# Kernel tuning notes

Measured on AMD Instinct MI355X. Metric: run time of the kernel, lower is better.

## Reference

```python
import jax, jax.numpy as jnp
import numpy as np

N = 100000   # nodes (batched graph)
E = 1600000  # edges
G = 2048     # molecules in the batch
D_IN = 128
D_H = 128
MLP_H = 512


def setup_inputs() -> dict:
    key = jax.random.key(0)
    ks = jax.random.split(key, 20)

    def w(k, i, o):
        return (jax.random.normal(k, (i, o), jnp.float32) / np.sqrt(i)).astype(jnp.float32)

    feats = jax.random.normal(ks[0], (N, D_IN), jnp.float32)
    src = jax.random.randint(ks[1], (E,), 0, N)
    dst = jax.random.randint(ks[2], (E,), 0, N)
    graph_ids = jnp.sort(jax.random.randint(ks[3], (N,), 0, G))

    return {
        "feats": feats, "src": src, "dst": dst, "graph_ids": graph_ids,
        # 3 GraphConv layers
        "W0": w(ks[4], D_IN, D_H), "b0": jnp.zeros((D_H,), jnp.float32),
        "W1": w(ks[5], D_H, D_H),  "b1": jnp.zeros((D_H,), jnp.float32),
        "W2": w(ks[6], D_H, D_H),  "b2": jnp.zeros((D_H,), jnp.float32),
        # MLP head: D_H -> 512 -> 256 -> 1
        "Wm0": w(ks[7], D_H, MLP_H),       "bm0": jnp.zeros((MLP_H,), jnp.float32),
        "Wm1": w(ks[8], MLP_H, MLP_H // 2), "bm1": jnp.zeros((MLP_H // 2,), jnp.float32),
        "Wm2": w(ks[9], MLP_H // 2, 1),     "bm2": jnp.zeros((1,), jnp.float32),
    }


def reference(feats, src, dst, graph_ids, W0, b0, W1, b1, W2, b2,
              Wm0, bm0, Wm1, bm1, Wm2, bm2):
    ones_e = jnp.ones((E,), jnp.float32)
    # DGL GraphConv norm='both': D_out^{-1/2} on src, D_in^{-1/2} on dst; deg clamped to 1
    deg_out = jnp.maximum(jax.ops.segment_sum(ones_e, src, num_segments=N), 1.0)
    deg_in = jnp.maximum(jax.ops.segment_sum(ones_e, dst, num_segments=N), 1.0)
    inv_src = jax.lax.rsqrt(deg_out)[:, None]
    inv_dst = jax.lax.rsqrt(deg_in)[:, None]

    def gcn_layer(h, W, b):
        h = h * inv_src                                   # [N, D]
        m = jax.ops.segment_sum(h[src], dst, num_segments=N)  # gather-scatter over edges
        m = m * inv_dst
        return jax.nn.relu(jnp.dot(m, W) + b)

    h = gcn_layer(feats, W0, b0)
    h = gcn_layer(h, W1, b1)
    h = gcn_layer(h, W2, b2)

    # AvgPooling per graph
    counts = jnp.maximum(jax.ops.segment_sum(jnp.ones((N,), jnp.float32), graph_ids, num_segments=G), 1.0)
    emb = jax.ops.segment_sum(h, graph_ids, num_segments=G) / counts[:, None]  # [G, D_H]

    # MLP head (dropout = identity in eval)
    x = jax.nn.relu(jnp.dot(emb, Wm0) + bm0)
    x = jax.nn.relu(jnp.dot(x, Wm1) + bm1)
    return jnp.dot(x, Wm2) + bm2  # [G, 1]
```

## Files before the change

### kernel.cpp

```cpp
#include <hip/hip_runtime.h>


static inline int ceil_div(int a, int b){ return (a + b - 1) / b; }

#define B1 256
#define NBMAX 1024

typedef __bf16 bf16x8 __attribute__((ext_vector_type(8)));
typedef float  f32x4  __attribute__((ext_vector_type(4)));

static __device__ inline __bf16 bits_to_bf16(unsigned short u){
  union { unsigned short u; __bf16 b; } x; x.u = u; return x.b;
}
static __device__ inline unsigned short bf16_bits(__bf16 b){
  union { __bf16 b; unsigned short u; } x; x.b = b; return x.u;
}
static __device__ inline unsigned pack_split(float s){
  __bf16 h = (__bf16)s;
  __bf16 l = (__bf16)(s - (float)h);
  return ((unsigned)bf16_bits(h) << 16) | (unsigned)bf16_bits(l);
}

__global__ __launch_bounds__(256) void bucket_count_kernel(
    const int* __restrict__ src, const int* __restrict__ dst,
    unsigned* __restrict__ cntA, unsigned* __restrict__ cntB,
    int E, int NB){
  __shared__ unsigned la[NBMAX], lb[NBMAX];
  int t = threadIdx.x;
  for (int i = t; i < NB; i += 256){ la[i] = 0u; lb[i] = 0u; }
  __syncthreads();
  int chunk = (E + B1 - 1) / B1;
  int e0 = blockIdx.x * chunk, e1 = min(e0 + chunk, E);
  for (int e = e0 + t; e < e1; e += 256){
    atomicAdd(&la[dst[e] >> 7], 1u);
    atomicAdd(&lb[src[e] >> 7], 1u);
  }
  __syncthreads();
  for (int i = t; i < NB; i += 256){
    cntA[(size_t)blockIdx.x * NB + i] = la[i];
    cntB[(size_t)blockIdx.x * NB + i] = lb[i];
  }
}

__global__ void scan_cols_kernel(unsigned* __restrict__ cntA, unsigned* __restrict__ cntB,
                                 unsigned* __restrict__ totals, int NB){
  int b = blockIdx.x * 256 + threadIdx.x;
  if (b >= NB) return;
  unsigned* cnt = blockIdx.y ? cntB : cntA;
  unsigned run = 0;
  for (int blk = 0; blk < B1; blk++){
    unsigned v = cnt[(size_t)blk * NB + b];
    cnt[(size_t)blk * NB + b] = run;
    run += v;
  }
  totals[(size_t)blockIdx.y * NB + b] = run;
}

__global__ void scan_base_kernel(const unsigned* __restrict__ totals,
                                 unsigned* __restrict__ baseA, unsigned* __restrict__ baseB,
                                 int NB, int E){
  __shared__ unsigned s[NBMAX];
  int t = threadIdx.x;
  for (int job = 0; job < 2; job++){
    unsigned* base = job ? baseB : baseA;
    unsigned x = (t < NB) ? totals[(size_t)job * NB + t] : 0u;
    s[t] = x;
    __syncthreads();
    for (int off = 1; off < NBMAX; off <<= 1){
      unsigned v = (t >= off) ? s[t - off] : 0u;
      __syncthreads();
      s[t] += v;
      __syncthreads();
    }
    if (t < NB) base[t] = s[t] - x;
    if (t == 0) base[NB] = (unsigned)E;
    __syncthreads();
  }
}

__global__ __launch_bounds__(256) void bucket_scatter_kernel(
    const int* __restrict__ src, const int* __restrict__ dst,
    const unsigned* __restrict__ cntA, const unsigned* __restrict__ cntB,
    const unsigned* __restrict__ baseA, const unsigned* __restrict__ baseB,
    unsigned* __restrict__ bpack_d, unsigned char* __restrict__ bsrc_s,
    int E, int NB){
  __shared__ unsigned curA[NBMAX], curB[NBMAX];
  int t = threadIdx.x;
  for (int i = t; i < NB; i += 256){
    curA[i] = baseA[i] + cntA[(size_t)blockIdx.x * NB + i];
    curB[i] = baseB[i] + cntB[(size_t)blockIdx.x * NB + i];
  }
  __syncthreads();
  int chunk = (E + B1 - 1) / B1;
  int e0 = blockIdx.x * chunk, e1 = min(e0 + chunk, E);
  for (int e = e0 + t; e < e1; e += 256){
    int s = src[e], d = dst[e];
    unsigned p = atomicAdd(&curA[d >> 7], 1u);
    bpack_d[p] = ((unsigned)(d & 127) << 17) | (unsigned)s;
    unsigned q = atomicAdd(&curB[s >> 7], 1u);
    bsrc_s[q] = (unsigned char)(s & 127);
  }
}

__global__ __launch_bounds__(256) void csr_finalize_kernel(
    const unsigned* __restrict__ bpack_d, const unsigned char* __restrict__ bsrc_s,
    const unsigned* __restrict__ baseA, const unsigned* __restrict__ baseB,
    int* __restrict__ row_ptr, float* __restrict__ inv_dst, float* __restrict__ inv_src,
    int* __restrict__ col, int N, int E, int NB){
  __shared__ unsigned cnt[128];
  __shared__ unsigned scn[128];
  int b = blockIdx.x, t = threadIdx.x;
  int node0 = b << 7;
  int nn = min(128, N - node0);
  int e0 = (int)baseA[b], e1 = (int)baseA[b + 1];
  if (t < 128) cnt[t] = 0u;
  __syncthreads();
  for (int e = e0 + t; e < e1; e += 256)
    atomicAdd(&cnt[(bpack_d[e] >> 17) & 127u], 1u);
  __syncthreads();
  unsigned mycnt = (t < 128) ? cnt[t] : 0u;
  if (t < 128) scn[t] = mycnt;
  __syncthreads();
  for (int off = 1; off < 128; off <<= 1){
    unsigned v = (t < 128 && t >= off) ? scn[t - off] : 0u;
    __syncthreads();
    if (t < 128) scn[t] += v;
    __syncthreads();
  }
  if (t < nn){
    unsigned excl = scn[t] - mycnt;
    row_ptr[node0 + t] = e0 + (int)excl;
    unsigned c = mycnt < 1u ? 1u : mycnt;
    inv_dst[node0 + t] = rsqrtf((float)c);
    cnt[t] = (unsigned)e0 + excl;
  }
  if (b == NB - 1 && t == 0) row_ptr[N] = E;
  __syncthreads();
  for (int e = e0 + t; e < e1; e += 256){
    unsigned v = bpack_d[e];
    unsigned p = atomicAdd(&cnt[(v >> 17) & 127u], 1u);
    col[p] = (int)(v & 0x1FFFFu);
  }
  __syncthreads();
  if (t < 128) cnt[t] = 0u;
  __syncthreads();
  int f0 = (int)baseB[b], f1 = (int)baseB[b + 1];
  for (int e = f0 + t; e < f1; e += 256)
    atomicAdd(&cnt[bsrc_s[e]], 1u);
  __syncthreads();
  if (t < nn){
    unsigned c = cnt[t] < 1u ? 1u : cnt[t];
    inv_src[node0 + t] = rsqrtf((float)c);
  }
}

template<bool SC>
__global__ __launch_bounds__(256) void csr_agg_kernel(
    const int* __restrict__ row_ptr, const int* __restrict__ col,
    const float* __restrict__ hs, const float* __restrict__ scale,
    const float* __restrict__ inv_dst, unsigned* __restrict__ aggp, int N){
  int node = (int)((blockIdx.x*256u + threadIdx.x) >> 5);
  int lane = threadIdx.x & 31;
  if (node >= N) return;
  int r0 = row_ptr[node];
  int r1 = row_ptr[node+1];
  float4 a0 = make_float4(0.f,0.f,0.f,0.f);
  float4 a1 = make_float4(0.f,0.f,0.f,0.f);
  float4 a2 = make_float4(0.f,0.f,0.f,0.f);
  float4 a3 = make_float4(0.f,0.f,0.f,0.f);
  int e = r0;
  for (; e + 3 < r1; e += 4){
    int s0 = col[e], s1 = col[e+1], s2 = col[e+2], s3 = col[e+3];
    float4 v0 = ((const float4*)(hs + (size_t)s0*128))[lane];
    float4 v1 = ((const float4*)(hs + (size_t)s1*128))[lane];
    float4 v2 = ((const float4*)(hs + (size_t)s2*128))[lane];
    float4 v3 = ((const float4*)(hs + (size_t)s3*128))[lane];
    if (SC){
      float c0 = scale[s0], c1 = scale[s1], c2 = scale[s2], c3 = scale[s3];
      v0.x*=c0; v0.y*=c0; v0.z*=c0; v0.w*=c0;
      v1.x*=c1; v1.y*=c1; v1.z*=c1; v1.w*=c1;
      v2.x*=c2; v2.y*=c2; v2.z*=c2; v2.w*=c2;
      v3.x*=c3; v3.y*=c3; v3.z*=c3; v3.w*=c3;
    }
    a0.x += v0.x; a0.y += v0.y; a0.z += v0.z; a0.w += v0.w;
    a1.x += v1.x; a1.y += v1.y; a1.z += v1.z; a1.w += v1.w;
    a2.x += v2.x; a2.y += v2.y; a2.z += v2.z; a2.w += v2.w;
    a3.x += v3.x; a3.y += v3.y; a3.z += v3.z; a3.w += v3.w;
  }
  for (; e < r1; e++){
    int s0 = col[e];
    float4 v0 = ((const float4*)(hs + (size_t)s0*128))[lane];
    if (SC){ float c0 = scale[s0]; v0.x*=c0; v0.y*=c0; v0.z*=c0; v0.w*=c0; }
    a0.x += v0.x; a0.y += v0.y; a0.z += v0.z; a0.w += v0.w;
  }
  float idst = inv_dst[node];
  float rx = ((a0.x + a1.x) + (a2.x + a3.x)) * idst;
  float ry = ((a0.y + a1.y) + (a2.y + a3.y)) * idst;
  float rz = ((a0.z + a1.z) + (a2.z + a3.z)) * idst;
  float rw = ((a0.w + a1.w) + (a2.w + a3.w)) * idst;
  uint4 p;
  p.x = pack_split(rx); p.y = pack_split(ry);
  p.z = pack_split(rz); p.w = pack_split(rw);
  ((uint4*)(aggp + (size_t)node*128))[lane] = p;
}

__global__ void wprep_kernel(const float* __restrict__ W0, const float* __restrict__ W1,
                             const float* __restrict__ W2,
                             __bf16* __restrict__ Wsp){
  int gidx = blockIdx.x*256 + threadIdx.x;
  if (gidx >= 3*128*128) return;
  int layer = gidx >> 14, idx = gidx & 16383;
  const float* W = layer == 0 ? W0 : (layer == 1 ? W1 : W2);
  int k = idx >> 7, n = idx & 127;
  float w = W[idx];
  __bf16 h = (__bf16)w;
  __bf16 l = (__bf16)(w - (float)h);
  Wsp[(size_t)layer*2*16384 + n*128 + k] = h;
  Wsp[(size_t)layer*2*16384 + 16384 + n*128 + k] = l;
}

__global__ __launch_bounds__(256) void mfma_gemm_kernel(
    const unsigned* __restrict__ A,
    const __bf16* __restrict__ Whi, const __bf16* __restrict__ Wlo,
    const float* __restrict__ bias, const float* __restrict__ out_scale,
    float* __restrict__ out, int M){
  const int tid  = threadIdx.x;
  const int wv   = tid >> 6;
  const int lane = tid & 63;
  const int q    = lane >> 4;
  const int mn   = lane & 15;
  const int row0 = blockIdx.x*128 + wv*32;

  f32x4 acc[2][8];
  #pragma unroll
  for (int mt = 0; mt < 2; mt++)
    #pragma unroll
    for (int nt = 0; nt < 8; nt++)
      acc[mt][nt] = (f32x4){0.f,0.f,0.f,0.f};

  #pragma unroll
  for (int kc = 0; kc < 4; kc++){
    bf16x8 ah[2], al[2];
    #pragma unroll
    for (int mt = 0; mt < 2; mt++){
      const unsigned* ap = A + (size_t)(row0 + mt*16 + mn)*128 + kc*32 + q*8;
      uint4 x0 = *(const uint4*)ap;
      uint4 x1 = *(const uint4*)(ap + 4);
      unsigned v[8] = {x0.x, x0.y, x0.z, x0.w, x1.x, x1.y, x1.z, x1.w};
      #pragma unroll
      for (int j = 0; j < 8; j++){
        ah[mt][j] = bits_to_bf16((unsigned short)(v[j] >> 16));
        al[mt][j] = bits_to_bf16((unsigned short)(v[j] & 0xFFFFu));
      }
    }
    #pragma unroll
    for (int nt = 0; nt < 8; nt++){
      size_t boff = (size_t)(nt*16 + mn)*128 + kc*32 + q*8;
      bf16x8 bh = *(const bf16x8*)(Whi + boff);
      bf16x8 bl = *(const bf16x8*)(Wlo + boff);
      #pragma unroll
      for (int mt = 0; mt < 2; mt++){
        acc[mt][nt] = __builtin_amdgcn_mfma_f32_16x16x32_bf16(al[mt], bh, acc[mt][nt], 0, 0, 0);
        acc[mt][nt] = __builtin_amdgcn_mfma_f32_16x16x32_bf16(ah[mt], bl, acc[mt][nt], 0, 0, 0);
        acc[mt][nt] = __builtin_amdgcn_mfma_f32_16x16x32_bf16(ah[mt], bh, acc[mt][nt], 0, 0, 0);
      }
    }
  }

  #pragma unroll
  for (int mt = 0; mt < 2; mt++){
    #pragma unroll
    for (int r = 0; r < 4; r++){
      int gm = row0 + mt*16 + q*4 + r;
      if (gm < M){
        float osc = out_scale ? out_scale[gm] : 1.f;
        #pragma unroll
        for (int nt = 0; nt < 8; nt++){
          float v = acc[mt][nt][r] + bias[nt*16 + mn];
          v = fmaxf(v, 0.f) * osc;
          out[(size_t)gm*128 + nt*16 + mn] = v;
        }
      }
    }
  }
}

__global__ __launch_bounds__(256) void gemm_kernel(
    const float* __restrict__ A, const float* __restrict__ W,
    const float* __restrict__ bias, const float* __restrict__ row_scale,
    const float* __restrict__ out_scale, float* __restrict__ out,
    int M, int K, int Ncols, int do_relu){
  __shared__ float As[32][68];
  __shared__ float Bs[32][128];

  const int tid = threadIdx.x;
  const int tx = tid & 31;
  const int ty = tid >> 5;
  const int row0 = blockIdx.x * 64;
  const int col0 = blockIdx.y * 128;

  float acc[8][4];
  #pragma unroll
  for (int i = 0; i < 8; i++)
    #pragma unroll
    for (int j = 0; j < 4; j++) acc[i][j] = 0.f;

  for (int kb = 0; kb < K; kb += 32){
    #pragma unroll
    for (int i = 0; i < 2; i++){
      int flat = i*256 + tid;
      int m = flat >> 3, k4 = (flat & 7) << 2;
      int gm = row0 + m;
      float4 v = make_float4(0.f, 0.f, 0.f, 0.f);
      if (gm < M){
        v = *(const float4*)(A + (size_t)gm*K + kb + k4);
        if (row_scale){ float s = row_scale[gm]; v.x*=s; v.y*=s; v.z*=s; v.w*=s; }
      }
      As[k4+0][m] = v.x; As[k4+1][m] = v.y; As[k4+2][m] = v.z; As[k4+3][m] = v.w;
    }
    #pragma unroll
    for (int i = 0; i < 4; i++){
      int flat = i*256 + tid;
      int k = flat >> 5, j4 = (flat & 31) << 2;
      float4 v = *(const float4*)(W + (size_t)(kb + k)*Ncols + col0 + j4);
      *(float4*)&Bs[k][j4] = v;
    }
    __syncthreads();
    #pragma unroll
    for (int k = 0; k < 32; k++){
      float4 b = *(const float4*)&Bs[k][tx << 2];
      float a[8];
      #pragma unroll
      for (int i = 0; i < 8; i++) a[i] = As[k][ty*8 + i];
      #pragma unroll
      for (int i = 0; i < 8; i++){
        acc[i][0] = fmaf(a[i], b.x, acc[i][0]);
        acc[i][1] = fmaf(a[i], b.y, acc[i][1]);
        acc[i][2] = fmaf(a[i], b.z, acc[i][2]);
        acc[i][3] = fmaf(a[i], b.w, acc[i][3]);
      }
    }
    __syncthreads();
  }

  float4 bi = *(const float4*)(bias + col0 + (tx << 2));
  #pragma unroll
  for (int i = 0; i < 8; i++){
    int gm = row0 + ty*8 + i;
    if (gm < M){
      float4 v;
      v.x = acc[i][0] + bi.x; v.y = acc[i][1] + bi.y;
      v.z = acc[i][2] + bi.z; v.w = acc[i][3] + bi.w;
      if (do_relu){
        v.x = fmaxf(v.x, 0.f); v.y = fmaxf(v.y, 0.f);
        v.z = fmaxf(v.z, 0.f); v.w = fmaxf(v.w, 0.f);
      }
      if (out_scale){ float s = out_scale[gm]; v.x*=s; v.y*=s; v.z*=s; v.w*=s; }
      *(float4*)(out + (size_t)gm*Ncols + col0 + (tx << 2)) = v;
    }
  }
}

__global__ void pool_kernel(const float* __restrict__ h, const int* __restrict__ gid,
                            float* __restrict__ emb, int N, int G){
  int g = blockIdx.x;
  int lane = threadIdx.x;
  int lo = 0, hi = N;
  while (lo < hi){ int mid = (lo + hi) >> 1; if (gid[mid] < g) lo = mid + 1; else hi = mid; }
  int start = lo;
  hi = N;
  while (lo < hi){ int mid = (lo + hi) >> 1; if (gid[mid] <= g) lo = mid + 1; else hi = mid; }
  int end = lo;
  float ax = 0.f, ay = 0.f;
  for (int n = start; n < end; n++){
    float2 v = ((const float2*)(h + (size_t)n*128))[lane];
    ax += v.x; ay += v.y;
  }
  int c = end - start; if (c < 1) c = 1;
  float invc = 1.0f / (float)c;
  float2 r; r.x = ax * invc; r.y = ay * invc;
  ((float2*)(emb + (size_t)g*128))[lane] = r;
}

__global__ void final_dot_kernel(const float* __restrict__ x, const float* __restrict__ w,
                                 const float* __restrict__ b, float* __restrict__ out, int G){
  int idx = blockIdx.x*blockDim.x + threadIdx.x;
  int g = idx >> 6, lane = idx & 63;
  if (g >= G) return;
  float4 xv = ((const float4*)(x + (size_t)g*256))[lane];
  float4 wv = ((const float4*)w)[lane];
  float s = xv.x*wv.x + xv.y*wv.y + xv.z*wv.z + xv.w*wv.w;
  for (int off = 32; off > 0; off >>= 1) s += __shfl_down(s, off);
  if (lane == 0) out[g] = s + b[0];
}

extern "C" void kernel_launch(void* const* d_in, const int* in_sizes, int n_in,
                              void* d_out, int out_size, void* d_ws, size_t ws_size,
                              hipStream_t stream){
  const float* feats = (const float*)d_in[0];
  const int*   src   = (const int*)d_in[1];
  const int*   dst   = (const int*)d_in[2];
  const int*   gid   = (const int*)d_in[3];
  const float* W0 = (const float*)d_in[4];   const float* b0 = (const float*)d_in[5];
  const float* W1 = (const float*)d_in[6];   const float* b1 = (const float*)d_in[7];
  const float* W2 = (const float*)d_in[8];   const float* b2 = (const float*)d_in[9];
  const float* Wm0 = (const float*)d_in[10]; const float* bm0 = (const float*)d_in[11];
  const float* Wm1 = (const float*)d_in[12]; const float* bm1 = (const float*)d_in[13];
  const float* Wm2 = (const float*)d_in[14]; const float* bm2 = (const float*)d_in[15];
  float* out = (float*)d_out;

  const int E   = in_sizes[1];
  const int N   = in_sizes[3];
  const int G   = out_size;
  const int MH  = in_sizes[11];
  const int MH2 = in_sizes[13];
  const int NB  = ceil_div(N, 128);

  char* ws = (char*)d_ws;
  size_t off = 0;
  auto carve = [&](size_t bytes) -> char* {
    off = (off + 255) & ~(size_t)255;
    char* p = ws + off; off += bytes; return p;
  };
  float* inv_src = (float*)carve((size_t)N*4);
  float* inv_dst = (float*)carve((size_t)N*4);
  int* row_ptr = (int*)carve((size_t)(N+1)*4);
  int* col     = (int*)carve((size_t)E*4);
  __bf16* Wsp = (__bf16*)carve(6*128*128*2);
  float* hs  = (float*)carve((size_t)N*128*4);
  unsigned* aggp = (unsigned*)carve((size_t)N*128*4);
  float* emb = (float*)carve((size_t)G*128*4);
  float* x1  = (float*)carve((size_t)G*MH*4);
  float* x2  = (float*)carve((size_t)G*MH2*4);

  unsigned* T = (unsigned*)aggp;
  unsigned* cntA   = T;
  unsigned* cntB   = cntA + (size_t)B1*NB;
  unsigned* totals = cntB + (size_t)B1*NB;
  unsigned* baseA  = totals + 2*(size_t)NB;
  unsigned* baseB  = baseA + (NB+1);
  unsigned* bpack_d = baseB + (NB+1);
  unsigned char* bsrc_s = (unsigned char*)(bpack_d + E);

  bucket_count_kernel<<<B1, 256, 0, stream>>>(src, dst, cntA, cntB, E, NB);
  scan_cols_kernel<<<dim3(ceil_div(NB,256), 2), 256, 0, stream>>>(cntA, cntB, totals, NB);
  scan_base_kernel<<<1, NBMAX, 0, stream>>>(totals, baseA, baseB, NB, E);
  bucket_scatter_kernel<<<B1, 256, 0, stream>>>(src, dst, cntA, cntB, baseA, baseB,
                                                bpack_d, bsrc_s, E, NB);
  csr_finalize_kernel<<<NB, 256, 0, stream>>>(bpack_d, bsrc_s, baseA, baseB,
                                              row_ptr, inv_dst, inv_src, col, N, E, NB);
  wprep_kernel<<<192, 256, 0, stream>>>(W0, W1, W2, Wsp);

  const int agg_blocks = ceil_div(N*32, 256);
  const int ggrid = ceil_div(N, 128);
  __bf16 *Whi0 = Wsp,            *Wlo0 = Wsp + 16384;
  __bf16 *Whi1 = Wsp + 2*16384,  *Wlo1 = Wsp + 3*16384;
  __bf16 *Whi2 = Wsp + 4*16384,  *Wlo2 = Wsp + 5*16384;
  csr_agg_kernel<true><<<agg_blocks, 256, 0, stream>>>(row_ptr, col, feats, inv_src, inv_dst, aggp, N);
  mfma_gemm_kernel<<<ggrid, 256, 0, stream>>>(aggp, Whi0, Wlo0, b0, inv_src, hs, N);
  csr_agg_kernel<false><<<agg_blocks, 256, 0, stream>>>(row_ptr, col, hs, nullptr, inv_dst, aggp, N);
  mfma_gemm_kernel<<<ggrid, 256, 0, stream>>>(aggp, Whi1, Wlo1, b1, inv_src, hs, N);
  csr_agg_kernel<false><<<agg_blocks, 256, 0, stream>>>(row_ptr, col, hs, nullptr, inv_dst, aggp, N);
  mfma_gemm_kernel<<<ggrid, 256, 0, stream>>>(aggp, Whi2, Wlo2, b2, nullptr, hs, N);
  pool_kernel<<<G, 64, 0, stream>>>(hs, gid, emb, N, G);
  gemm_kernel<<<dim3(ceil_div(G,64), MH/128),  256, 0, stream>>>(emb, Wm0, bm0, nullptr, nullptr, x1, G, 128, MH, 1);
  gemm_kernel<<<dim3(ceil_div(G,64), MH2/128), 256, 0, stream>>>(x1, Wm1, bm1, nullptr, nullptr, x2, G, MH, MH2, 1);
  final_dot_kernel<<<ceil_div(G*64,256), 256, 0, stream>>>(x2, Wm2, bm2, out, G);
}
```

Before: 789.7 us.

## Stage edge buckets in LDS per chunk and fuse pooling with MLP head

The count and scatter passes of CSR construction are merged into one kernel. Each block sorts its edge chunk into per-bucket order in shared memory and writes the staged chunk contiguously, and the finalize kernel reads each chunk's segment using the per-block offsets. Weight preparation rides along as extra blocks of that kernel, and pooling plus the three MLP layers become a single head kernel that handles 8 graphs per block. This removes several launches and one full pass over the edge list, at the cost of serial per-thread loops in finalize and a smaller, less parallel head GEMM.

```diff
diff --git a/kernel.cpp b/kernel.cpp
--- a/kernel.cpp
+++ b/kernel.cpp
@@ -5,6 +5,8 @@
 
 #define B1 256
 #define NBMAX 1024
+#define CHUNK_MAX 7168
+#define WPREP_BLOCKS 192
 
 typedef __bf16 bf16x8 __attribute__((ext_vector_type(8)));
 typedef float  f32x4  __attribute__((ext_vector_type(4)));
@@ -21,39 +23,105 @@
   return ((unsigned)bf16_bits(h) << 16) | (unsigned)bf16_bits(l);
 }
 
-__global__ __launch_bounds__(256) void bucket_count_kernel(
+__global__ __launch_bounds__(256) void scatter_count_kernel(
     const int* __restrict__ src, const int* __restrict__ dst,
     unsigned* __restrict__ cntA, unsigned* __restrict__ cntB,
+    unsigned* __restrict__ stagedA, unsigned char* __restrict__ stagedB,
+    const float* __restrict__ W0, const float* __restrict__ W1,
+    const float* __restrict__ W2, __bf16* __restrict__ Wsp,
     int E, int NB){
+  if (blockIdx.x >= B1){
+    int gidx = (blockIdx.x - B1)*256 + threadIdx.x;
+    if (gidx < 3*128*128){
+      int layer = gidx >> 14, idx = gidx & 16383;
+      const float* W = layer == 0 ? W0 : (layer == 1 ? W1 : W2);
+      int k = idx >> 7, n = idx & 127;
+      float w = W[idx];
+      __bf16 h = (__bf16)w;
+      __bf16 l = (__bf16)(w - (float)h);
+      Wsp[(size_t)layer*2*16384 + n*128 + k] = h;
+      Wsp[(size_t)layer*2*16384 + 16384 + n*128 + k] = l;
+    }
+    return;
+  }
+
   __shared__ unsigned la[NBMAX], lb[NBMAX];
-  int t = threadIdx.x;
-  for (int i = t; i < NB; i += 256){ la[i] = 0u; lb[i] = 0u; }
-  __syncthreads();
-  int chunk = (E + B1 - 1) / B1;
-  int e0 = blockIdx.x * chunk, e1 = min(e0 + chunk, E);
+  __shared__ unsigned tsum[256];
+  __shared__ unsigned stA[CHUNK_MAX];
+  __shared__ unsigned char stB[CHUNK_MAX];
+
+  const int t = threadIdx.x;
+  const int blk = blockIdx.x;
+  const int chunk = (E + B1 - 1) / B1;
+  const int e0 = blk * chunk, e1 = min(e0 + chunk, E);
+  const int len = e1 - e0;
+  const int strideB = (chunk + 3) & ~3;
+
+  #pragma unroll
+  for (int i = t; i < NBMAX; i += 256){ la[i] = 0u; lb[i] = 0u; }
+  __syncthreads();
   for (int e = e0 + t; e < e1; e += 256){
     atomicAdd(&la[dst[e] >> 7], 1u);
     atomicAdd(&lb[src[e] >> 7], 1u);
   }
   __syncthreads();
-  for (int i = t; i < NB; i += 256){
-    cntA[(size_t)blockIdx.x * NB + i] = la[i];
-    cntB[(size_t)blockIdx.x * NB + i] = lb[i];
-  }
-}
-
-__global__ void scan_cols_kernel(unsigned* __restrict__ cntA, unsigned* __restrict__ cntB,
-                                 unsigned* __restrict__ totals, int NB){
+
+  for (int job = 0; job < 2; job++){
+    unsigned* lx = job ? lb : la;
+    unsigned* cx = job ? cntB : cntA;
+    int b4 = t*4;
+    unsigned v0 = lx[b4], v1 = lx[b4+1], v2 = lx[b4+2], v3 = lx[b4+3];
+    unsigned s = v0+v1+v2+v3;
+    tsum[t] = s;
+    __syncthreads();
+    for (int off = 1; off < 256; off <<= 1){
+      unsigned u = (t >= off) ? tsum[t-off] : 0u;
+      __syncthreads();
+      tsum[t] += u;
+      __syncthreads();
+    }
+    unsigned run = tsum[t] - s;
+    unsigned o0 = run, o1 = run+v0, o2 = run+v0+v1, o3 = run+v0+v1+v2;
+    lx[b4] = o0; lx[b4+1] = o1; lx[b4+2] = o2; lx[b4+3] = o3;
+    if (b4   < NB) cx[(size_t)blk*NB + b4  ] = o0;
+    if (b4+1 < NB) cx[(size_t)blk*NB + b4+1] = o1;
+    if (b4+2 < NB) cx[(size_t)blk*NB + b4+2] = o2;
+    if (b4+3 < NB) cx[(size_t)blk*NB + b4+3] = o3;
+    __syncthreads();
+  }
+
+  for (int e = e0 + t; e < e1; e += 256){
+    int s = src[e], d = dst[e];
+    unsigned pA = atomicAdd(&la[d >> 7], 1u);
+    stA[pA] = ((unsigned)(d & 127) << 17) | (unsigned)s;
+    unsigned pB = atomicAdd(&lb[s >> 7], 1u);
+    stB[pB] = (unsigned char)(s & 127);
+  }
+  __syncthreads();
+
+  for (int i = t; i < len; i += 256)
+    stagedA[(size_t)blk*chunk + i] = stA[i];
+  int w4 = (len + 3) >> 2;
+  unsigned* gB = (unsigned*)(stagedB + (size_t)blk*strideB);
+  for (int i = t; i < w4; i += 256)
+    gB[i] = *(unsigned*)&stB[4*i];
+}
+
+__global__ void totals_kernel(const unsigned* __restrict__ cntA,
+                              const unsigned* __restrict__ cntB,
+                              unsigned* __restrict__ totals, int NB, int E){
   int b = blockIdx.x * 256 + threadIdx.x;
   if (b >= NB) return;
-  unsigned* cnt = blockIdx.y ? cntB : cntA;
+  const unsigned* cx = blockIdx.y ? cntB : cntA;
+  const int chunk = (E + B1 - 1) / B1;
   unsigned run = 0;
   for (int blk = 0; blk < B1; blk++){
-    unsigned v = cnt[(size_t)blk * NB + b];
-    cnt[(size_t)blk * NB + b] = run;
-    run += v;
-  }
-  totals[(size_t)blockIdx.y * NB + b] = run;
+    int lenb = E - blk*chunk; if (lenb > chunk) lenb = chunk; if (lenb < 0) lenb = 0;
+    unsigned cur = cx[(size_t)blk*NB + b];
+    unsigned nxt = (b < NB-1) ? cx[(size_t)blk*NB + b + 1] : (unsigned)lenb;
+    run += nxt - cur;
+  }
+  totals[(size_t)blockIdx.y*NB + b] = run;
 }
 
 __global__ void scan_base_kernel(const unsigned* __restrict__ totals,
@@ -63,7 +131,7 @@
   int t = threadIdx.x;
   for (int job = 0; job < 2; job++){
     unsigned* base = job ? baseB : baseA;
-    unsigned x = (t < NB) ? totals[(size_t)job * NB + t] : 0u;
+    unsigned x = (t < NB) ? totals[(size_t)job*NB + t] : 0u;
     s[t] = x;
     __syncthreads();
     for (int off = 1; off < NBMAX; off <<= 1){
@@ -78,45 +146,29 @@
   }
 }
 
-__global__ __launch_bounds__(256) void bucket_scatter_kernel(
-    const int* __restrict__ src, const int* __restrict__ dst,
+__global__ __launch_bounds__(256) void csr_finalize_kernel(
+    const unsigned* __restrict__ stagedA, const unsigned char* __restrict__ stagedB,
     const unsigned* __restrict__ cntA, const unsigned* __restrict__ cntB,
-    const unsigned* __restrict__ baseA, const unsigned* __restrict__ baseB,
-    unsigned* __restrict__ bpack_d, unsigned char* __restrict__ bsrc_s,
-    int E, int NB){
-  __shared__ unsigned curA[NBMAX], curB[NBMAX];
-  int t = threadIdx.x;
-  for (int i = t; i < NB; i += 256){
-    curA[i] = baseA[i] + cntA[(size_t)blockIdx.x * NB + i];
-    curB[i] = baseB[i] + cntB[(size_t)blockIdx.x * NB + i];
-  }
-  __syncthreads();
-  int chunk = (E + B1 - 1) / B1;
-  int e0 = blockIdx.x * chunk, e1 = min(e0 + chunk, E);
-  for (int e = e0 + t; e < e1; e += 256){
-    int s = src[e], d = dst[e];
-    unsigned p = atomicAdd(&curA[d >> 7], 1u);
-    bpack_d[p] = ((unsigned)(d & 127) << 17) | (unsigned)s;
-    unsigned q = atomicAdd(&curB[s >> 7], 1u);
-    bsrc_s[q] = (unsigned char)(s & 127);
-  }
-}
-
-__global__ __launch_bounds__(256) void csr_finalize_kernel(
-    const unsigned* __restrict__ bpack_d, const unsigned char* __restrict__ bsrc_s,
-    const unsigned* __restrict__ baseA, const unsigned* __restrict__ baseB,
+    const unsigned* __restrict__ baseA,
     int* __restrict__ row_ptr, float* __restrict__ inv_dst, float* __restrict__ inv_src,
     int* __restrict__ col, int N, int E, int NB){
   __shared__ unsigned cnt[128];
   __shared__ unsigned scn[128];
-  int b = blockIdx.x, t = threadIdx.x;
-  int node0 = b << 7;
-  int nn = min(128, N - node0);
-  int e0 = (int)baseA[b], e1 = (int)baseA[b + 1];
+  const int b = blockIdx.x, t = threadIdx.x;
+  const int node0 = b << 7;
+  const int nn = min(128, N - node0);
+  const int chunk = (E + B1 - 1) / B1;
+  const int strideB = (chunk + 3) & ~3;
+  int lenb = E - t*chunk; if (lenb > chunk) lenb = chunk; if (lenb < 0) lenb = 0;
+
+  const unsigned a0 = cntA[(size_t)t*NB + b];
+  const unsigned a1 = (b < NB-1) ? cntA[(size_t)t*NB + b + 1] : (unsigned)lenb;
+  const unsigned* segA = stagedA + (size_t)t*chunk;
+
   if (t < 128) cnt[t] = 0u;
   __syncthreads();
-  for (int e = e0 + t; e < e1; e += 256)
-    atomicAdd(&cnt[(bpack_d[e] >> 17) & 127u], 1u);
+  for (unsigned i = a0; i < a1; i++)
+    atomicAdd(&cnt[(segA[i] >> 17) & 127u], 1u);
   __syncthreads();
   unsigned mycnt = (t < 128) ? cnt[t] : 0u;
   if (t < 128) scn[t] = mycnt;
@@ -127,6 +179,7 @@
     if (t < 128) scn[t] += v;
     __syncthreads();
   }
+  int e0 = (int)baseA[b];
   if (t < nn){
     unsigned excl = scn[t] - mycnt;
     row_ptr[node0 + t] = e0 + (int)excl;
@@ -136,17 +189,19 @@
   }
   if (b == NB - 1 && t == 0) row_ptr[N] = E;
   __syncthreads();
-  for (int e = e0 + t; e < e1; e += 256){
-    unsigned v = bpack_d[e];
+  for (unsigned i = a0; i < a1; i++){
+    unsigned v = segA[i];
     unsigned p = atomicAdd(&cnt[(v >> 17) & 127u], 1u);
     col[p] = (int)(v & 0x1FFFFu);
   }
   __syncthreads();
   if (t < 128) cnt[t] = 0u;
   __syncthreads();
-  int f0 = (int)baseB[b], f1 = (int)baseB[b + 1];
-  for (int e = f0 + t; e < f1; e += 256)
-    atomicAdd(&cnt[bsrc_s[e]], 1u);
+  const unsigned b0o = cntB[(size_t)t*NB + b];
+  const unsigned b1o = (b < NB-1) ? cntB[(size_t)t*NB + b + 1] : (unsigned)lenb;
+  const unsigned char* segB = stagedB + (size_t)t*strideB;
+  for (unsigned i = b0o; i < b1o; i++)
+    atomicAdd(&cnt[segB[i]], 1u);
   __syncthreads();
   if (t < nn){
     unsigned c = cnt[t] < 1u ? 1u : cnt[t];
@@ -204,21 +259,6 @@
   ((uint4*)(aggp + (size_t)node*128))[lane] = p;
 }
 
-__global__ void wprep_kernel(const float* __restrict__ W0, const float* __restrict__ W1,
-                             const float* __restrict__ W2,
-                             __bf16* __restrict__ Wsp){
-  int gidx = blockIdx.x*256 + threadIdx.x;
-  if (gidx >= 3*128*128) return;
-  int layer = gidx >> 14, idx = gidx & 16383;
-  const float* W = layer == 0 ? W0 : (layer == 1 ? W1 : W2);
-  int k = idx >> 7, n = idx & 127;
-  float w = W[idx];
-  __bf16 h = (__bf16)w;
-  __bf16 l = (__bf16)(w - (float)h);
-  Wsp[(size_t)layer*2*16384 + n*128 + k] = h;
-  Wsp[(size_t)layer*2*16384 + 16384 + n*128 + k] = l;
-}
-
 __global__ __launch_bounds__(256) void mfma_gemm_kernel(
     const unsigned* __restrict__ A,
     const __bf16* __restrict__ Whi, const __bf16* __restrict__ Wlo,
@@ -285,113 +325,93 @@
   }
 }
 
-__global__ __launch_bounds__(256) void gemm_kernel(
-    const float* __restrict__ A, const float* __restrict__ W,
-    const float* __restrict__ bias, const float* __restrict__ row_scale,
-    const float* __restrict__ out_scale, float* __restrict__ out,
-    int M, int K, int Ncols, int do_relu){
-  __shared__ float As[32][68];
-  __shared__ float Bs[32][128];
-
-  const int tid = threadIdx.x;
-  const int tx = tid & 31;
-  const int ty = tid >> 5;
-  const int row0 = blockIdx.x * 64;
-  const int col0 = blockIdx.y * 128;
-
-  float acc[8][4];
-  #pragma unroll
-  for (int i = 0; i < 8; i++)
-    #pragma unroll
-    for (int j = 0; j < 4; j++) acc[i][j] = 0.f;
-
-  for (int kb = 0; kb < K; kb += 32){
-    #pragma unroll
-    for (int i = 0; i < 2; i++){
-      int flat = i*256 + tid;
-      int m = flat >> 3, k4 = (flat & 7) << 2;
-      int gm = row0 + m;
-      float4 v = make_float4(0.f, 0.f, 0.f, 0.f);
-      if (gm < M){
-        v = *(const float4*)(A + (size_t)gm*K + kb + k4);
-        if (row_scale){ float s = row_scale[gm]; v.x*=s; v.y*=s; v.z*=s; v.w*=s; }
+__global__ __launch_bounds__(256) void head_kernel(
+    const float* __restrict__ h, const int* __restrict__ gid,
+    const float* __restrict__ Wm0, const float* __restrict__ bm0,
+    const float* __restrict__ Wm1, const float* __restrict__ bm1,
+    const float* __restrict__ Wm2, const float* __restrict__ bm2,
+    float* __restrict__ out, int N, int G){
+  __shared__ float embL[8][128];
+  __shared__ float x1L[8][512];
+  __shared__ float x2L[8][256];
+
+  const int t = threadIdx.x;
+  const int wave = t >> 6, lane = t & 63;
+  const int g0 = blockIdx.x * 8;
+
+  for (int gg = 0; gg < 2; gg++){
+    int gl = wave*2 + gg;
+    int g = g0 + gl;
+    float ax = 0.f, ay = 0.f;
+    int start = 0, end = 0;
+    if (g < G){
+      int lo = 0, hi = N;
+      while (lo < hi){ int mid = (lo + hi) >> 1; if (gid[mid] < g) lo = mid + 1; else hi = mid; }
+      start = lo;
+      hi = N;
+      while (lo < hi){ int mid = (lo + hi) >> 1; if (gid[mid] <= g) lo = mid + 1; else hi = mid; }
+      end = lo;
+      for (int n = start; n < end; n++){
+        float2 v = ((const float2*)(h + (size_t)n*128))[lane];
+        ax += v.x; ay += v.y;
       }
-      As[k4+0][m] = v.x; As[k4+1][m] = v.y; As[k4+2][m] = v.z; As[k4+3][m] = v.w;
-    }
-    #pragma unroll
-    for (int i = 0; i < 4; i++){
-      int flat = i*256 + tid;
-      int k = flat >> 5, j4 = (flat & 31) << 2;
-      float4 v = *(const float4*)(W + (size_t)(kb + k)*Ncols + col0 + j4);
-      *(float4*)&Bs[k][j4] = v;
-    }
-    __syncthreads();
-    #pragma unroll
-    for (int k = 0; k < 32; k++){
-      float4 b = *(const float4*)&Bs[k][tx << 2];
-      float a[8];
+    }
+    int c = end - start; if (c < 1) c = 1;
+    float invc = 1.0f / (float)c;
+    embL[gl][2*lane]   = ax * invc;
+    embL[gl][2*lane+1] = ay * invc;
+  }
+  __syncthreads();
+
+  {
+    float acc[8][2];
+    #pragma unroll
+    for (int g = 0; g < 8; g++){ acc[g][0] = 0.f; acc[g][1] = 0.f; }
+    for (int k = 0; k < 128; k++){
+      float w0 = Wm0[(size_t)k*512 + t];
+      float w1 = Wm0[(size_t)k*512 + t + 256];
       #pragma unroll
-      for (int i = 0; i < 8; i++) a[i] = As[k][ty*8 + i];
+      for (int g = 0; g < 8; g++){
+        float e = embL[g][k];
+        acc[g][0] = fmaf(e, w0, acc[g][0]);
+        acc[g][1] = fmaf(e, w1, acc[g][1]);
+      }
+    }
+    float b0v = bm0[t], b1v = bm0[t + 256];
+    #pragma unroll
+    for (int g = 0; g < 8; g++){
+      x1L[g][t]       = fmaxf(acc[g][0] + b0v, 0.f);
+      x1L[g][t + 256] = fmaxf(acc[g][1] + b1v, 0.f);
+    }
+  }
+  __syncthreads();
+
+  {
+    float acc[8];
+    #pragma unroll
+    for (int g = 0; g < 8; g++) acc[g] = 0.f;
+    for (int k = 0; k < 512; k++){
+      float w = Wm1[(size_t)k*256 + t];
       #pragma unroll
-      for (int i = 0; i < 8; i++){
-        acc[i][0] = fmaf(a[i], b.x, acc[i][0]);
-        acc[i][1] = fmaf(a[i], b.y, acc[i][1]);
-        acc[i][2] = fmaf(a[i], b.z, acc[i][2]);
-        acc[i][3] = fmaf(a[i], b.w, acc[i][3]);
-      }
-    }
-    __syncthreads();
-  }
-
-  float4 bi = *(const float4*)(bias + col0 + (tx << 2));
-  #pragma unroll
-  for (int i = 0; i < 8; i++){
-    int gm = row0 + ty*8 + i;
-    if (gm < M){
-      float4 v;
-      v.x = acc[i][0] + bi.x; v.y = acc[i][1] + bi.y;
-      v.z = acc[i][2] + bi.z; v.w = acc[i][3] + bi.w;
-      if (do_relu){
-        v.x = fmaxf(v.x, 0.f); v.y = fmaxf(v.y, 0.f);
-        v.z = fmaxf(v.z, 0.f); v.w = fmaxf(v.w, 0.f);
-      }
-      if (out_scale){ float s = out_scale[gm]; v.x*=s; v.y*=s; v.z*=s; v.w*=s; }
-      *(float4*)(out + (size_t)gm*Ncols + col0 + (tx << 2)) = v;
-    }
-  }
-}
-
-__global__ void pool_kernel(const float* __restrict__ h, const int* __restrict__ gid,
-                            float* __restrict__ emb, int N, int G){
-  int g = blockIdx.x;
-  int lane = threadIdx.x;
-  int lo = 0, hi = N;
-  while (lo < hi){ int mid = (lo + hi) >> 1; if (gid[mid] < g) lo = mid + 1; else hi = mid; }
-  int start = lo;
-  hi = N;
-  while (lo < hi){ int mid = (lo + hi) >> 1; if (gid[mid] <= g) lo = mid + 1; else hi = mid; }
-  int end = lo;
-  float ax = 0.f, ay = 0.f;
-  for (int n = start; n < end; n++){
-    float2 v = ((const float2*)(h + (size_t)n*128))[lane];
-    ax += v.x; ay += v.y;
-  }
-  int c = end - start; if (c < 1) c = 1;
-  float invc = 1.0f / (float)c;
-  float2 r; r.x = ax * invc; r.y = ay * invc;
-  ((float2*)(emb + (size_t)g*128))[lane] = r;
-}
-
-__global__ void final_dot_kernel(const float* __restrict__ x, const float* __restrict__ w,
-                                 const float* __restrict__ b, float* __restrict__ out, int G){
-  int idx = blockIdx.x*blockDim.x + threadIdx.x;
-  int g = idx >> 6, lane = idx & 63;
-  if (g >= G) return;
-  float4 xv = ((const float4*)(x + (size_t)g*256))[lane];
-  float4 wv = ((const float4*)w)[lane];
-  float s = xv.x*wv.x + xv.y*wv.y + xv.z*wv.z + xv.w*wv.w;
-  for (int off = 32; off > 0; off >>= 1) s += __shfl_down(s, off);
-  if (lane == 0) out[g] = s + b[0];
+      for (int g = 0; g < 8; g++)
+        acc[g] = fmaf(x1L[g][k], w, acc[g]);
+    }
+    float bv = bm1[t];
+    #pragma unroll
+    for (int g = 0; g < 8; g++)
+      x2L[g][t] = fmaxf(acc[g] + bv, 0.f);
+  }
+  __syncthreads();
+
+  {
+    int g = t >> 5;
+    int c = t & 31;
+    float s = 0.f;
+    for (int i = c; i < 256; i += 32)
+      s = fmaf(x2L[g][i], Wm2[i], s);
+    for (int off = 16; off > 0; off >>= 1) s += __shfl_down(s, off, 32);
+    if (c == 0 && (g0 + g) < G) out[g0 + g] = s + bm2[0];
+  }
 }
 
 extern "C" void kernel_launch(void* const* d_in, const int* in_sizes, int n_in,
@@ -412,9 +432,9 @@
   const int E   = in_sizes[1];
   const int N   = in_sizes[3];
   const int G   = out_size;
-  const int MH  = in_sizes[11];
-  const int MH2 = in_sizes[13];
   const int NB  = ceil_div(N, 128);
+  const int chunk = ceil_div(E, B1);
+  const int strideB = (chunk + 3) & ~3;
 
   char* ws = (char*)d_ws;
   size_t off = 0;
@@ -429,9 +449,6 @@
   __bf16* Wsp = (__bf16*)carve(6*128*128*2);
   float* hs  = (float*)carve((size_t)N*128*4);
   unsigned* aggp = (unsigned*)carve((size_t)N*128*4);
-  float* emb = (float*)carve((size_t)G*128*4);
-  float* x1  = (float*)carve((size_t)G*MH*4);
-  float* x2  = (float*)carve((size_t)G*MH2*4);
 
   unsigned* T = (unsigned*)aggp;
   unsigned* cntA   = T;
@@ -439,17 +456,15 @@
   unsigned* totals = cntB + (size_t)B1*NB;
   unsigned* baseA  = totals + 2*(size_t)NB;
   unsigned* baseB  = baseA + (NB+1);
-  unsigned* bpack_d = baseB + (NB+1);
-  unsigned char* bsrc_s = (unsigned char*)(bpack_d + E);
-
-  bucket_count_kernel<<<B1, 256, 0, stream>>>(src, dst, cntA, cntB, E, NB);
-  scan_cols_kernel<<<dim3(ceil_div(NB,256), 2), 256, 0, stream>>>(cntA, cntB, totals, NB);
+  unsigned* stagedA = baseB + (NB+1);
+  unsigned char* stagedB = (unsigned char*)(stagedA + (size_t)B1*chunk);
+
+  scatter_count_kernel<<<B1 + WPREP_BLOCKS, 256, 0, stream>>>(
+      src, dst, cntA, cntB, stagedA, stagedB, W0, W1, W2, Wsp, E, NB);
+  totals_kernel<<<dim3(ceil_div(NB,256), 2), 256, 0, stream>>>(cntA, cntB, totals, NB, E);
   scan_base_kernel<<<1, NBMAX, 0, stream>>>(totals, baseA, baseB, NB, E);
-  bucket_scatter_kernel<<<B1, 256, 0, stream>>>(src, dst, cntA, cntB, baseA, baseB,
-                                                bpack_d, bsrc_s, E, NB);
-  csr_finalize_kernel<<<NB, 256, 0, stream>>>(bpack_d, bsrc_s, baseA, baseB,
+  csr_finalize_kernel<<<NB, 256, 0, stream>>>(stagedA, stagedB, cntA, cntB, baseA,
                                               row_ptr, inv_dst, inv_src, col, N, E, NB);
-  wprep_kernel<<<192, 256, 0, stream>>>(W0, W1, W2, Wsp);
 
   const int agg_blocks = ceil_div(N*32, 256);
   const int ggrid = ceil_div(N, 128);
@@ -462,8 +477,5 @@
   mfma_gemm_kernel<<<ggrid, 256, 0, stream>>>(aggp, Whi1, Wlo1, b1, inv_src, hs, N);
   csr_agg_kernel<false><<<agg_blocks, 256, 0, stream>>>(row_ptr, col, hs, nullptr, inv_dst, aggp, N);
   mfma_gemm_kernel<<<ggrid, 256, 0, stream>>>(aggp, Whi2, Wlo2, b2, nullptr, hs, N);
-  pool_kernel<<<G, 64, 0, stream>>>(hs, gid, emb, N, G);
-  gemm_kernel<<<dim3(ceil_div(G,64), MH/128),  256, 0, stream>>>(emb, Wm0, bm0, nullptr, nullptr, x1, G, 128, MH, 1);
-  gemm_kernel<<<dim3(ceil_div(G,64), MH2/128), 256, 0, stream>>>(x1, Wm1, bm1, nullptr, nullptr, x2, G, MH, MH2, 1);
-  final_dot_kernel<<<ceil_div(G*64,256), 256, 0, stream>>>(x2, Wm2, bm2, out, G);
-}
+  head_kernel<<<ceil_div(G,8), 256, 0, stream>>>(hs, gid, Wm0, bm0, Wm1, bm1, Wm2, bm2, out, N, G);
+}
```

Result: no change. 775.3 us (-1.8%).
